# Kernel optimization log

Hardware: AMD Instinct MI355X
Metric: run time of the kernel (lower is better)

Reference implementation:

```python
import jax, jax.numpy as jnp
import numpy as np

B, H, S, D = 4, 16, 2048, 64

def setup_inputs() -> dict:
    key = jax.random.key(0)
    kq, kk, kv = jax.random.split(key, 3)
    q = jax.random.normal(kq, (B, H, S, D), dtype=jnp.float32)
    k = jax.random.normal(kk, (B, H, S, D), dtype=jnp.float32)
    v = jax.random.normal(kv, (B, H, S, D), dtype=jnp.float32)
    # broadcastable causal mask: True = attend
    mask = jnp.tril(jnp.ones((S, S), dtype=bool))[None, None, :, :]
    return {"q": q, "k": k, "v": v, "mask": mask}

def reference(q, k, v, mask):
    # qk = einsum('... q d, ... k d -> ... q k'); mask -> -inf; softmax(qk/sqrt(d_k)); @ v
    scale = 1.0 / jnp.sqrt(jnp.asarray(q.shape[-1], q.dtype))
    scores = jnp.einsum('bhqd,bhkd->bhqk', q, k)
    scores = jnp.where(mask, scores, -jnp.inf) * scale  # -inf * scale stays -inf
    attn = jax.nn.softmax(scores, axis=-1)
    return jnp.einsum('bhqk,bhkd->bhqd', attn, v)
```

## Files before the change

### kernel.cpp

```cpp
#include <hip/hip_runtime.h>


#define SEQ 2048
#define HD  64

typedef __attribute__((ext_vector_type(8))) short short8;
typedef __attribute__((ext_vector_type(4))) float f32x4;

__device__ __forceinline__ unsigned f2bfu(float f) {
    union { float f; unsigned u; } x; x.f = f;
    return (x.u + 0x7fff + ((x.u >> 16) & 1)) >> 16;
}
__device__ __forceinline__ unsigned pk2(float lo, float hi) {
    return f2bfu(lo) | (f2bfu(hi) << 16);
}

__global__ __launch_bounds__(256, 2) void sdpa_kernel(
    const float* __restrict__ Q, const float* __restrict__ K,
    const float* __restrict__ V, float* __restrict__ O)
{
    __shared__ __align__(16) char smraw[32768];

    const int bx = blockIdx.x;
    const int qt = 15 - (bx >> 6);
    const int bh = bx & 63;
    const int qbase = qt * 128;

    const int tid  = threadIdx.x;
    const int lane = tid & 63;
    const int w    = tid >> 6;
    const int g    = lane >> 4;
    const int r16  = lane & 15;
    const int wq   = qbase + w * 32;

    const size_t base = (size_t)bh * (SEQ * HD);

    const float SC = 0.18033688011112042f;
    short8 qf[2][2];
    #pragma unroll
    for (int qs = 0; qs < 2; ++qs) {
        const float* qp = Q + base + (size_t)(wq + qs * 16 + r16) * HD + 8 * g;
        #pragma unroll
        for (int c = 0; c < 2; ++c) {
            f32x4 a = *(const f32x4*)(qp + c * 32);
            f32x4 b = *(const f32x4*)(qp + c * 32 + 4);
            union { short8 s; unsigned u[4]; } t;
            t.u[0] = pk2(a[0] * SC, a[1] * SC);
            t.u[1] = pk2(a[2] * SC, a[3] * SC);
            t.u[2] = pk2(b[0] * SC, b[1] * SC);
            t.u[3] = pk2(b[2] * SC, b[3] * SC);
            qf[qs][c] = t.s;
        }
    }

    f32x4 oacc[2][4] = {};
    float mrun[2] = {-1e30f, -1e30f};
    float lrun[2] = {0.0f, 0.0f};

    const int k_kvo = tid >> 2;
    const int k_o   = k_kvo & 31;
    const int k_row = (k_kvo & 32) + 16 * ((k_o >> 2) & 1) + 4 * (k_o >> 3) + (k_o & 3);
    const int k_dc  = (tid & 3) * 2;
    const int v_kv0 = (tid & 31) * 2;
    const int v_db  = (tid >> 5) * 8;

    f32x4 ka0, ka1, kb0, kb1, va0, va1, vb0, vb1;

    auto LOADT = [&](int kvbase) {
        const float* kp = K + base + (size_t)(kvbase + k_kvo) * HD + k_dc * 8;
        ka0 = *(const f32x4*)(kp + 0);
        ka1 = *(const f32x4*)(kp + 4);
        kb0 = *(const f32x4*)(kp + 8);
        kb1 = *(const f32x4*)(kp + 12);
        const float* vp = V + base + (size_t)(kvbase + v_kv0) * HD + v_db;
        va0 = *(const f32x4*)(vp + 0);
        va1 = *(const f32x4*)(vp + 4);
        vb0 = *(const f32x4*)(vp + HD);
        vb1 = *(const f32x4*)(vp + HD + 4);
    };
    auto WRITET = [&](int b) {
        char* Kl = smraw + b * 16384;
        char* Vl = Kl + 8192;
        union { short8 s; unsigned u[4]; } c0, c1;
        c0.u[0] = pk2(ka0[0], ka0[1]); c0.u[1] = pk2(ka0[2], ka0[3]);
        c0.u[2] = pk2(ka1[0], ka1[1]); c0.u[3] = pk2(ka1[2], ka1[3]);
        c1.u[0] = pk2(kb0[0], kb0[1]); c1.u[1] = pk2(kb0[2], kb0[3]);
        c1.u[2] = pk2(kb1[0], kb1[1]); c1.u[3] = pk2(kb1[2], kb1[3]);
        const int r7 = k_row & 7;
        *(short8*)(Kl + ((k_row * 8 + (k_dc ^ r7)) << 4))       = c0.s;
        *(short8*)(Kl + ((k_row * 8 + ((k_dc + 1) ^ r7)) << 4)) = c1.s;
        const int u  = v_kv0 >> 3;
        const int wo = (v_kv0 & 7) * 2;
        #pragma unroll
        for (int i = 0; i < 4; ++i) {
            const int d = v_db + i;
            *(unsigned*)(Vl + ((d * 8 + (u ^ (d & 7))) << 4) + wo) = pk2(va0[i], vb0[i]);
        }
        #pragma unroll
        for (int i = 0; i < 4; ++i) {
            const int d = v_db + 4 + i;
            *(unsigned*)(Vl + ((d * 8 + (u ^ (d & 7))) << 4) + wo) = pk2(va1[i], vb1[i]);
        }
    };

    const int nkvb = (qbase + 128) >> 6;

    LOADT(0);
    WRITET(0);
    __syncthreads();

    for (int kvb = 0; kvb < nkvb; ++kvb) {
        const int kvbase = kvb << 6;
        const int buf = kvb & 1;
        const bool more = (kvb + 1 < nkvb);

        if (more) LOADT((kvb + 1) << 6);

        if (kvbase <= wq + 31) {
            const char* Kl = smraw + buf * 16384;
            const char* Vl = Kl + 8192;

            f32x4 sa[2][2][2];
            #pragma unroll
            for (int qs = 0; qs < 2; ++qs)
                #pragma unroll
                for (int c2 = 0; c2 < 2; ++c2)
                    #pragma unroll
                    for (int t = 0; t < 2; ++t)
                        sa[qs][c2][t] = (f32x4){0.f, 0.f, 0.f, 0.f};
            __builtin_amdgcn_s_setprio(1);
            #pragma unroll
            for (int c2 = 0; c2 < 2; ++c2)
                #pragma unroll
                for (int t = 0; t < 2; ++t)
                    #pragma unroll
                    for (int c = 0; c < 2; ++c) {
                        const int row = c2 * 32 + t * 16 + r16;
                        short8 kf = *(const short8*)(Kl + ((row * 8 + ((4 * c + g) ^ (row & 7))) << 4));
                        sa[0][c2][t] = __builtin_amdgcn_mfma_f32_16x16x32_bf16(kf, qf[0][c], sa[0][c2][t], 0, 0, 0);
                        sa[1][c2][t] = __builtin_amdgcn_mfma_f32_16x16x32_bf16(kf, qf[1][c], sa[1][c2][t], 0, 0, 0);
                    }
            __builtin_amdgcn_s_setprio(0);

            #pragma unroll
            for (int qs = 0; qs < 2; ++qs) {
                const int q0 = wq + qs * 16;
                if (kvbase + 63 > q0) {
                    const int qrow = q0 + r16;
                    #pragma unroll
                    for (int c2 = 0; c2 < 2; ++c2)
                        #pragma unroll
                        for (int t = 0; t < 2; ++t)
                            #pragma unroll
                            for (int r = 0; r < 4; ++r) {
                                const int kv = kvbase + c2 * 32 + 8 * g + 4 * t + r;
                                if (kv > qrow) sa[qs][c2][t][r] = -1e30f;
                            }
                }
            }

            float mnew[2];
            #pragma unroll
            for (int qs = 0; qs < 2; ++qs) {
                float mloc = sa[qs][0][0][0];
                #pragma unroll
                for (int c2 = 0; c2 < 2; ++c2)
                    #pragma unroll
                    for (int t = 0; t < 2; ++t)
                        #pragma unroll
                        for (int r = 0; r < 4; ++r)
                            mloc = fmaxf(mloc, sa[qs][c2][t][r]);
                mloc = fmaxf(mloc, __shfl_xor(mloc, 16));
                mloc = fmaxf(mloc, __shfl_xor(mloc, 32));
                mnew[qs] = fmaxf(mrun[qs], mloc);
            }
            if (!__all((mnew[0] - mrun[0] <= 8.0f) && (mnew[1] - mrun[1] <= 8.0f))) {
                #pragma unroll
                for (int qs = 0; qs < 2; ++qs) {
                    const float alpha = __builtin_amdgcn_exp2f(mrun[qs] - mnew[qs]);
                    lrun[qs] *= alpha;
                    mrun[qs] = mnew[qs];
                    #pragma unroll
                    for (int dt = 0; dt < 4; ++dt) oacc[qs][dt] *= alpha;
                }
            }
            #pragma unroll
            for (int qs = 0; qs < 2; ++qs) {
                float ls = 0.0f;
                #pragma unroll
                for (int c2 = 0; c2 < 2; ++c2)
                    #pragma unroll
                    for (int t = 0; t < 2; ++t)
                        #pragma unroll
                        for (int r = 0; r < 4; ++r) {
                            const float p = __builtin_amdgcn_exp2f(sa[qs][c2][t][r] - mrun[qs]);
                            sa[qs][c2][t][r] = p;
                            ls += p;
                        }
                ls += __shfl_xor(ls, 16);
                ls += __shfl_xor(ls, 32);
                lrun[qs] += ls;
            }

            #pragma unroll
            for (int c2 = 0; c2 < 2; ++c2) {
                union { short8 s; unsigned u[4]; } pf0, pf1;
                pf0.u[0] = pk2(sa[0][c2][0][0], sa[0][c2][0][1]);
                pf0.u[1] = pk2(sa[0][c2][0][2], sa[0][c2][0][3]);
                pf0.u[2] = pk2(sa[0][c2][1][0], sa[0][c2][1][1]);
                pf0.u[3] = pk2(sa[0][c2][1][2], sa[0][c2][1][3]);
                pf1.u[0] = pk2(sa[1][c2][0][0], sa[1][c2][0][1]);
                pf1.u[1] = pk2(sa[1][c2][0][2], sa[1][c2][0][3]);
                pf1.u[2] = pk2(sa[1][c2][1][0], sa[1][c2][1][1]);
                pf1.u[3] = pk2(sa[1][c2][1][2], sa[1][c2][1][3]);
                __builtin_amdgcn_s_setprio(1);
                #pragma unroll
                for (int dt = 0; dt < 4; ++dt) {
                    const int row = dt * 16 + r16;
                    short8 vf = *(const short8*)(Vl + ((row * 8 + ((c2 * 4 + g) ^ (row & 7))) << 4));
                    oacc[0][dt] = __builtin_amdgcn_mfma_f32_16x16x32_bf16(vf, pf0.s, oacc[0][dt], 0, 0, 0);
                    oacc[1][dt] = __builtin_amdgcn_mfma_f32_16x16x32_bf16(vf, pf1.s, oacc[1][dt], 0, 0, 0);
                }
                __builtin_amdgcn_s_setprio(0);
            }
        }

        if (more) {
            WRITET(buf ^ 1);
            __syncthreads();
        }
    }

    #pragma unroll
    for (int qs = 0; qs < 2; ++qs) {
        const float inv = 1.0f / lrun[qs];
        float* op = O + base + (size_t)(wq + qs * 16 + r16) * HD + 4 * g;
        #pragma unroll
        for (int dt = 0; dt < 4; ++dt) {
            f32x4 vv = oacc[qs][dt] * inv;
            *(f32x4*)(op + dt * 16) = vv;
        }
    }
}

extern "C" void kernel_launch(void* const* d_in, const int* in_sizes, int n_in,
                              void* d_out, int out_size, void* d_ws, size_t ws_size,
                              hipStream_t stream) {
    (void)in_sizes; (void)n_in; (void)out_size; (void)d_ws; (void)ws_size;
    const float* q = (const float*)d_in[0];
    const float* k = (const float*)d_in[1];
    const float* v = (const float*)d_in[2];
    float* o = (float*)d_out;
    sdpa_kernel<<<dim3(64 * 16), dim3(256), 0, stream>>>(q, k, v, o);
}
```

Measured before the change: 202.2 us.

## Pair causal query tiles per block, compute row sums via MFMA, use native bf16 convert

Each block now handles two query tiles (15-p and p), so every block does the same amount of causal work, and the grid shrinks to 512 blocks. The softmax row sum is now accumulated with an extra MFMA against a ones vector instead of scalar adds and cross-lane shuffles. The manual bf16 rounding is replaced by the compiler's vector float-to-bf16 conversion. In exchange, half as many blocks may leave CUs underused, the two tiles run serially within a block, and the row sum is built from bf16-rounded probabilities.

Result: faster. 183.7 us (-9.2%).

```diff
diff --git a/kernel.cpp b/kernel.cpp
--- a/kernel.cpp
+++ b/kernel.cpp
@@ -6,13 +6,13 @@
 
 typedef __attribute__((ext_vector_type(8))) short short8;
 typedef __attribute__((ext_vector_type(4))) float f32x4;
-
-__device__ __forceinline__ unsigned f2bfu(float f) {
-    union { float f; unsigned u; } x; x.f = f;
-    return (x.u + 0x7fff + ((x.u >> 16) & 1)) >> 16;
-}
+typedef __attribute__((ext_vector_type(2))) float f32x2;
+typedef __attribute__((ext_vector_type(2))) __bf16 bf16x2;
+
 __device__ __forceinline__ unsigned pk2(float lo, float hi) {
-    return f2bfu(lo) | (f2bfu(hi) << 16);
+    union { bf16x2 v; unsigned u; } r;
+    r.v = __builtin_convertvector((f32x2){lo, hi}, bf16x2);
+    return r.u;
 }
 
 __global__ __launch_bounds__(256, 2) void sdpa_kernel(
@@ -22,40 +22,16 @@
     __shared__ __align__(16) char smraw[32768];
 
     const int bx = blockIdx.x;
-    const int qt = 15 - (bx >> 6);
+    const int p  = bx >> 6;
     const int bh = bx & 63;
-    const int qbase = qt * 128;
 
     const int tid  = threadIdx.x;
     const int lane = tid & 63;
     const int w    = tid >> 6;
     const int g    = lane >> 4;
     const int r16  = lane & 15;
-    const int wq   = qbase + w * 32;
 
     const size_t base = (size_t)bh * (SEQ * HD);
-
-    const float SC = 0.18033688011112042f;
-    short8 qf[2][2];
-    #pragma unroll
-    for (int qs = 0; qs < 2; ++qs) {
-        const float* qp = Q + base + (size_t)(wq + qs * 16 + r16) * HD + 8 * g;
-        #pragma unroll
-        for (int c = 0; c < 2; ++c) {
-            f32x4 a = *(const f32x4*)(qp + c * 32);
-            f32x4 b = *(const f32x4*)(qp + c * 32 + 4);
-            union { short8 s; unsigned u[4]; } t;
-            t.u[0] = pk2(a[0] * SC, a[1] * SC);
-            t.u[1] = pk2(a[2] * SC, a[3] * SC);
-            t.u[2] = pk2(b[0] * SC, b[1] * SC);
-            t.u[3] = pk2(b[2] * SC, b[3] * SC);
-            qf[qs][c] = t.s;
-        }
-    }
-
-    f32x4 oacc[2][4] = {};
-    float mrun[2] = {-1e30f, -1e30f};
-    float lrun[2] = {0.0f, 0.0f};
 
     const int k_kvo = tid >> 2;
     const int k_o   = k_kvo & 31;
@@ -63,6 +39,10 @@
     const int k_dc  = (tid & 3) * 2;
     const int v_kv0 = (tid & 31) * 2;
     const int v_db  = (tid >> 5) * 8;
+
+    short8 ones;
+    { union { short8 s; unsigned u[4]; } o_;
+      o_.u[0] = o_.u[1] = o_.u[2] = o_.u[3] = 0x3F803F80u; ones = o_.s; }
 
     f32x4 ka0, ka1, kb0, kb1, va0, va1, vb0, vb1;
 
@@ -103,142 +83,167 @@
         }
     };
 
-    const int nkvb = (qbase + 128) >> 6;
-
-    LOADT(0);
-    WRITET(0);
-    __syncthreads();
-
-    for (int kvb = 0; kvb < nkvb; ++kvb) {
-        const int kvbase = kvb << 6;
-        const int buf = kvb & 1;
-        const bool more = (kvb + 1 < nkvb);
-
-        if (more) LOADT((kvb + 1) << 6);
-
-        if (kvbase <= wq + 31) {
-            const char* Kl = smraw + buf * 16384;
-            const char* Vl = Kl + 8192;
-
-            f32x4 sa[2][2][2];
+    const float SC = 0.18033688011112042f;
+
+    #pragma unroll 1
+    for (int tile = 0; tile < 2; ++tile) {
+        const int qbase = (tile == 0 ? 15 - p : p) * 128;
+        const int wq = qbase + w * 32;
+
+        short8 qf[2][2];
+        #pragma unroll
+        for (int qs = 0; qs < 2; ++qs) {
+            const float* qp = Q + base + (size_t)(wq + qs * 16 + r16) * HD + 8 * g;
             #pragma unroll
-            for (int qs = 0; qs < 2; ++qs)
+            for (int c = 0; c < 2; ++c) {
+                f32x4 a = *(const f32x4*)(qp + c * 32);
+                f32x4 b = *(const f32x4*)(qp + c * 32 + 4);
+                union { short8 s; unsigned u[4]; } t;
+                t.u[0] = pk2(a[0] * SC, a[1] * SC);
+                t.u[1] = pk2(a[2] * SC, a[3] * SC);
+                t.u[2] = pk2(b[0] * SC, b[1] * SC);
+                t.u[3] = pk2(b[2] * SC, b[3] * SC);
+                qf[qs][c] = t.s;
+            }
+        }
+
+        f32x4 oacc[2][4] = {};
+        f32x4 lacc[2] = {};
+        float mrun[2] = {-1e30f, -1e30f};
+
+        const int nkvb = (qbase + 128) >> 6;
+
+        __syncthreads();
+        LOADT(0);
+        WRITET(0);
+        __syncthreads();
+
+        for (int kvb = 0; kvb < nkvb; ++kvb) {
+            const int kvbase = kvb << 6;
+            const int buf = kvb & 1;
+            const bool more = (kvb + 1 < nkvb);
+
+            if (more) LOADT((kvb + 1) << 6);
+
+            if (kvbase <= wq + 31) {
+                const char* Kl = smraw + buf * 16384;
+                const char* Vl = Kl + 8192;
+
+                f32x4 sa[2][2][2];
+                #pragma unroll
+                for (int qs = 0; qs < 2; ++qs)
+                    #pragma unroll
+                    for (int c2 = 0; c2 < 2; ++c2)
+                        #pragma unroll
+                        for (int t = 0; t < 2; ++t)
+                            sa[qs][c2][t] = (f32x4){0.f, 0.f, 0.f, 0.f};
+                __builtin_amdgcn_s_setprio(1);
                 #pragma unroll
                 for (int c2 = 0; c2 < 2; ++c2)
                     #pragma unroll
                     for (int t = 0; t < 2; ++t)
-                        sa[qs][c2][t] = (f32x4){0.f, 0.f, 0.f, 0.f};
-            __builtin_amdgcn_s_setprio(1);
-            #pragma unroll
-            for (int c2 = 0; c2 < 2; ++c2)
-                #pragma unroll
-                for (int t = 0; t < 2; ++t)
-                    #pragma unroll
-                    for (int c = 0; c < 2; ++c) {
-                        const int row = c2 * 32 + t * 16 + r16;
-                        short8 kf = *(const short8*)(Kl + ((row * 8 + ((4 * c + g) ^ (row & 7))) << 4));
-                        sa[0][c2][t] = __builtin_amdgcn_mfma_f32_16x16x32_bf16(kf, qf[0][c], sa[0][c2][t], 0, 0, 0);
-                        sa[1][c2][t] = __builtin_amdgcn_mfma_f32_16x16x32_bf16(kf, qf[1][c], sa[1][c2][t], 0, 0, 0);
+                        #pragma unroll
+                        for (int c = 0; c < 2; ++c) {
+                            const int row = c2 * 32 + t * 16 + r16;
+                            short8 kf = *(const short8*)(Kl + ((row * 8 + ((4 * c + g) ^ (row & 7))) << 4));
+                            sa[0][c2][t] = __builtin_amdgcn_mfma_f32_16x16x32_bf16(kf, qf[0][c], sa[0][c2][t], 0, 0, 0);
+                            sa[1][c2][t] = __builtin_amdgcn_mfma_f32_16x16x32_bf16(kf, qf[1][c], sa[1][c2][t], 0, 0, 0);
+                        }
+                __builtin_amdgcn_s_setprio(0);
+
+                #pragma unroll
+                for (int qs = 0; qs < 2; ++qs) {
+                    const int q0 = wq + qs * 16;
+                    if (kvbase + 63 > q0) {
+                        const int qrow = q0 + r16;
+                        #pragma unroll
+                        for (int c2 = 0; c2 < 2; ++c2)
+                            #pragma unroll
+                            for (int t = 0; t < 2; ++t)
+                                #pragma unroll
+                                for (int r = 0; r < 4; ++r) {
+                                    const int kv = kvbase + c2 * 32 + 8 * g + 4 * t + r;
+                                    if (kv > qrow) sa[qs][c2][t][r] = -1e30f;
+                                }
                     }
-            __builtin_amdgcn_s_setprio(0);
-
-            #pragma unroll
-            for (int qs = 0; qs < 2; ++qs) {
-                const int q0 = wq + qs * 16;
-                if (kvbase + 63 > q0) {
-                    const int qrow = q0 + r16;
+                }
+
+                float mnew[2];
+                #pragma unroll
+                for (int qs = 0; qs < 2; ++qs) {
+                    float mloc = sa[qs][0][0][0];
                     #pragma unroll
                     for (int c2 = 0; c2 < 2; ++c2)
                         #pragma unroll
                         for (int t = 0; t < 2; ++t)
                             #pragma unroll
-                            for (int r = 0; r < 4; ++r) {
-                                const int kv = kvbase + c2 * 32 + 8 * g + 4 * t + r;
-                                if (kv > qrow) sa[qs][c2][t][r] = -1e30f;
-                            }
-                }
-            }
-
-            float mnew[2];
+                            for (int r = 0; r < 4; ++r)
+                                mloc = fmaxf(mloc, sa[qs][c2][t][r]);
+                    mloc = fmaxf(mloc, __shfl_xor(mloc, 16));
+                    mloc = fmaxf(mloc, __shfl_xor(mloc, 32));
+                    mnew[qs] = fmaxf(mrun[qs], mloc);
+                }
+                if (!__all((mnew[0] - mrun[0] <= 8.0f) && (mnew[1] - mrun[1] <= 8.0f))) {
+                    #pragma unroll
+                    for (int qs = 0; qs < 2; ++qs) {
+                        const float alpha = __builtin_amdgcn_exp2f(mrun[qs] - mnew[qs]);
+                        mrun[qs] = mnew[qs];
+                        lacc[qs][0] *= alpha;
+                        #pragma unroll
+                        for (int dt = 0; dt < 4; ++dt) oacc[qs][dt] *= alpha;
+                    }
+                }
+                #pragma unroll
+                for (int qs = 0; qs < 2; ++qs)
+                    #pragma unroll
+                    for (int c2 = 0; c2 < 2; ++c2)
+                        #pragma unroll
+                        for (int t = 0; t < 2; ++t)
+                            #pragma unroll
+                            for (int r = 0; r < 4; ++r)
+                                sa[qs][c2][t][r] =
+                                    __builtin_amdgcn_exp2f(sa[qs][c2][t][r] - mrun[qs]);
+
+                #pragma unroll
+                for (int c2 = 0; c2 < 2; ++c2) {
+                    union { short8 s; unsigned u[4]; } pf0, pf1;
+                    pf0.u[0] = pk2(sa[0][c2][0][0], sa[0][c2][0][1]);
+                    pf0.u[1] = pk2(sa[0][c2][0][2], sa[0][c2][0][3]);
+                    pf0.u[2] = pk2(sa[0][c2][1][0], sa[0][c2][1][1]);
+                    pf0.u[3] = pk2(sa[0][c2][1][2], sa[0][c2][1][3]);
+                    pf1.u[0] = pk2(sa[1][c2][0][0], sa[1][c2][0][1]);
+                    pf1.u[1] = pk2(sa[1][c2][0][2], sa[1][c2][0][3]);
+                    pf1.u[2] = pk2(sa[1][c2][1][0], sa[1][c2][1][1]);
+                    pf1.u[3] = pk2(sa[1][c2][1][2], sa[1][c2][1][3]);
+                    __builtin_amdgcn_s_setprio(1);
+                    lacc[0] = __builtin_amdgcn_mfma_f32_16x16x32_bf16(ones, pf0.s, lacc[0], 0, 0, 0);
+                    lacc[1] = __builtin_amdgcn_mfma_f32_16x16x32_bf16(ones, pf1.s, lacc[1], 0, 0, 0);
+                    #pragma unroll
+                    for (int dt = 0; dt < 4; ++dt) {
+                        const int row = dt * 16 + r16;
+                        short8 vf = *(const short8*)(Vl + ((row * 8 + ((c2 * 4 + g) ^ (row & 7))) << 4));
+                        oacc[0][dt] = __builtin_amdgcn_mfma_f32_16x16x32_bf16(vf, pf0.s, oacc[0][dt], 0, 0, 0);
+                        oacc[1][dt] = __builtin_amdgcn_mfma_f32_16x16x32_bf16(vf, pf1.s, oacc[1][dt], 0, 0, 0);
+                    }
+                    __builtin_amdgcn_s_setprio(0);
+                }
+            }
+
+            if (more) {
+                WRITET(buf ^ 1);
+                __syncthreads();
+            }
+        }
+
+        #pragma unroll
+        for (int qs = 0; qs < 2; ++qs) {
+            const float inv = 1.0f / lacc[qs][0];
+            float* op = O + base + (size_t)(wq + qs * 16 + r16) * HD + 4 * g;
             #pragma unroll
-            for (int qs = 0; qs < 2; ++qs) {
-                float mloc = sa[qs][0][0][0];
-                #pragma unroll
-                for (int c2 = 0; c2 < 2; ++c2)
-                    #pragma unroll
-                    for (int t = 0; t < 2; ++t)
-                        #pragma unroll
-                        for (int r = 0; r < 4; ++r)
-                            mloc = fmaxf(mloc, sa[qs][c2][t][r]);
-                mloc = fmaxf(mloc, __shfl_xor(mloc, 16));
-                mloc = fmaxf(mloc, __shfl_xor(mloc, 32));
-                mnew[qs] = fmaxf(mrun[qs], mloc);
-            }
-            if (!__all((mnew[0] - mrun[0] <= 8.0f) && (mnew[1] - mrun[1] <= 8.0f))) {
-                #pragma unroll
-                for (int qs = 0; qs < 2; ++qs) {
-                    const float alpha = __builtin_amdgcn_exp2f(mrun[qs] - mnew[qs]);
-                    lrun[qs] *= alpha;
-                    mrun[qs] = mnew[qs];
-                    #pragma unroll
-                    for (int dt = 0; dt < 4; ++dt) oacc[qs][dt] *= alpha;
-                }
-            }
-            #pragma unroll
-            for (int qs = 0; qs < 2; ++qs) {
-                float ls = 0.0f;
-                #pragma unroll
-                for (int c2 = 0; c2 < 2; ++c2)
-                    #pragma unroll
-                    for (int t = 0; t < 2; ++t)
-                        #pragma unroll
-                        for (int r = 0; r < 4; ++r) {
-                            const float p = __builtin_amdgcn_exp2f(sa[qs][c2][t][r] - mrun[qs]);
-                            sa[qs][c2][t][r] = p;
-                            ls += p;
-                        }
-                ls += __shfl_xor(ls, 16);
-                ls += __shfl_xor(ls, 32);
-                lrun[qs] += ls;
-            }
-
-            #pragma unroll
-            for (int c2 = 0; c2 < 2; ++c2) {
-                union { short8 s; unsigned u[4]; } pf0, pf1;
-                pf0.u[0] = pk2(sa[0][c2][0][0], sa[0][c2][0][1]);
-                pf0.u[1] = pk2(sa[0][c2][0][2], sa[0][c2][0][3]);
-                pf0.u[2] = pk2(sa[0][c2][1][0], sa[0][c2][1][1]);
-                pf0.u[3] = pk2(sa[0][c2][1][2], sa[0][c2][1][3]);
-                pf1.u[0] = pk2(sa[1][c2][0][0], sa[1][c2][0][1]);
-                pf1.u[1] = pk2(sa[1][c2][0][2], sa[1][c2][0][3]);
-                pf1.u[2] = pk2(sa[1][c2][1][0], sa[1][c2][1][1]);
-                pf1.u[3] = pk2(sa[1][c2][1][2], sa[1][c2][1][3]);
-                __builtin_amdgcn_s_setprio(1);
-                #pragma unroll
-                for (int dt = 0; dt < 4; ++dt) {
-                    const int row = dt * 16 + r16;
-                    short8 vf = *(const short8*)(Vl + ((row * 8 + ((c2 * 4 + g) ^ (row & 7))) << 4));
-                    oacc[0][dt] = __builtin_amdgcn_mfma_f32_16x16x32_bf16(vf, pf0.s, oacc[0][dt], 0, 0, 0);
-                    oacc[1][dt] = __builtin_amdgcn_mfma_f32_16x16x32_bf16(vf, pf1.s, oacc[1][dt], 0, 0, 0);
-                }
-                __builtin_amdgcn_s_setprio(0);
-            }
-        }
-
-        if (more) {
-            WRITET(buf ^ 1);
-            __syncthreads();
-        }
-    }
-
-    #pragma unroll
-    for (int qs = 0; qs < 2; ++qs) {
-        const float inv = 1.0f / lrun[qs];
-        float* op = O + base + (size_t)(wq + qs * 16 + r16) * HD + 4 * g;
-        #pragma unroll
-        for (int dt = 0; dt < 4; ++dt) {
-            f32x4 vv = oacc[qs][dt] * inv;
-            *(f32x4*)(op + dt * 16) = vv;
+            for (int dt = 0; dt < 4; ++dt) {
+                f32x4 vv = oacc[qs][dt] * inv;
+                *(f32x4*)(op + dt * 16) = vv;
+            }
         }
     }
 }
@@ -251,5 +256,5 @@
     const float* k = (const float*)d_in[1];
     const float* v = (const float*)d_in[2];
     float* o = (float*)d_out;
-    sdpa_kernel<<<dim3(64 * 16), dim3(256), 0, stream>>>(q, k, v, o);
+    sdpa_kernel<<<dim3(64 * 8), dim3(256), 0, stream>>>(q, k, v, o);
 }
```
